# Optimization experiments

Hardware: AMD Instinct MI355X
Metric: run time of the kernel (lower is better)

The kernel has to match this reference:

```python
import jax, jax.numpy as jnp
import numpy as np

B = 256        # number of graphs
NPG = 256      # nodes per graph
N = B * NPG    # total nodes
F = 128        # node feature dim
DEG = 16       # avg degree
E = N * DEG    # total edges
LAT = [32, 32, 32, 1]
D = sum(LAT)   # total_latent_dim = 97
K = 30         # sortpool k
C1, C2, KW2 = 16, 32, 5
DENSE = ((K - 2) // 2 + 1 - KW2 + 1) * C2  # 352
OUT = 2


def setup_inputs() -> dict:
    key = jax.random.key(0)
    ks = jax.random.split(key, 16)
    node_feat = jax.random.normal(ks[0], (N, F), jnp.float32)
    # edges constrained within each graph (block-diagonal adjacency)
    base = ((jnp.arange(E, dtype=jnp.int32) // (E // B)) * NPG).astype(jnp.int32)
    src = jax.random.randint(ks[1], (E,), 0, NPG, dtype=jnp.int32) + base
    dst = jax.random.randint(ks[2], (E,), 0, NPG, dtype=jnp.int32) + base
    degs = jnp.zeros((N,), jnp.int32).at[dst].add(1)  # in-degree per node
    s = 0.1
    dims = [F] + LAT
    inp = {"node_feat": node_feat, "src": src, "dst": dst, "degs": degs}
    for i in range(4):
        inp[f"W{i}"] = jax.random.normal(ks[3 + i], (dims[i], dims[i + 1]), jnp.float32) * s
        inp[f"b{i}"] = jnp.zeros((dims[i + 1],), jnp.float32)
    inp["conv1_w"] = jax.random.normal(ks[8], (C1, 1, D), jnp.float32) * s
    inp["conv1_b"] = jnp.zeros((C1,), jnp.float32)
    inp["conv2_w"] = jax.random.normal(ks[9], (C2, C1, KW2), jnp.float32) * s
    inp["conv2_b"] = jnp.zeros((C2,), jnp.float32)
    inp["out_w"] = jax.random.normal(ks[10], (DENSE, OUT), jnp.float32) * s
    inp["out_b"] = jnp.zeros((OUT,), jnp.float32)
    return inp


def reference(node_feat, W0, b0, W1, b1, W2, b2, W3, b3,
              conv1_w, conv1_b, conv2_w, conv2_b, out_w, out_b,
              src, dst, degs):
    n = node_feat.shape[0]
    deg1 = (degs.astype(node_feat.dtype) + 1.0)[:, None]  # node_degs = deg + 1
    h = node_feat
    feats = []
    for W, b in ((W0, b0), (W1, b1), (W2, b2), (W3, b3)):
        # gnn_spmm(n2n, h) + h : sparse adjacency matmul via segment add
        pooled = jnp.zeros((n, h.shape[1]), h.dtype).at[dst].add(h[src]) + h
        h = jnp.tanh((pooled @ W + b) / deg1)
        feats.append(h)
    Z = jnp.concatenate(feats, axis=1)          # [N, D]
    Zb = Z.reshape(B, NPG, D)                   # equal-sized graphs
    # sortpooling: top-k on last latent channel per graph, gather rows
    _, idx = jax.lax.top_k(Zb[:, :, -1], K)     # [B, K]
    sp = jnp.take_along_axis(Zb, idx[:, :, None], axis=1)  # [B, K, D]
    x = sp.reshape(B, 1, K * D)
    dn = ('NCH', 'OIH', 'NCH')
    x = jax.lax.conv_general_dilated(x, conv1_w, (D,), 'VALID', dimension_numbers=dn)
    x = jax.nn.relu(x + conv1_b[None, :, None])          # [B, C1, K]
    x = x.reshape(B, C1, K // 2, 2).max(axis=-1)         # maxpool1d(2,2) -> [B, C1, 15]
    x = jax.lax.conv_general_dilated(x, conv2_w, (1,), 'VALID', dimension_numbers=dn)
    x = jax.nn.relu(x + conv2_b[None, :, None])          # [B, C2, 11]
    to_dense = x.reshape(B, -1)                          # [B, 352]
    out = jax.nn.relu(to_dense @ out_w + out_b)
    return jax.nn.relu(out)  # original applies conv1d_activation twice at the end
```

## Files before the change

### kernel.cpp

```cpp
#include <hip/hip_runtime.h>

#define NPG  256
#define EPG  4096
#define FDIM 128
#define KTOP 30

__global__ __launch_bounds__(256, 1)
void dgcnn_fused(const float* __restrict__ node_feat,
                 const int* __restrict__ srcv, const int* __restrict__ dstv,
                 const int* __restrict__ degs,
                 const float* __restrict__ W0, const float* __restrict__ b0,
                 const float* __restrict__ W1, const float* __restrict__ b1,
                 const float* __restrict__ W2, const float* __restrict__ b2,
                 const float* __restrict__ W3, const float* __restrict__ b3,
                 const float* __restrict__ cw1, const float* __restrict__ cb1,
                 const float* __restrict__ cw2, const float* __restrict__ cb2,
                 const float* __restrict__ ow,  const float* __restrict__ ob,
                 float* __restrict__ outp)
{
    __shared__ float Ybuf[NPG * 33];
    __shared__ int   srclist[EPG];
    __shared__ int   offs[NPG];
    __shared__ int   cnt [NPG];
    __shared__ int   degl[NPG];
    __shared__ float invd[NPG];
    __shared__ float keys[NPG];
    __shared__ int   sel [KTOP + 2];

    const int g = blockIdx.x;
    const int t = threadIdx.x;

    int dn = degs[g * NPG + t];
    degl[t] = dn;
    cnt[t]  = 0;
    invd[t] = 1.0f / (float)(dn + 1);
    offs[t] = dn;
    __syncthreads();
    for (int s = 1; s < NPG; s <<= 1) {
        int v = (t >= s) ? offs[t - s] : 0;
        __syncthreads();
        offs[t] += v;
        __syncthreads();
    }
    int excl = offs[t] - dn;
    __syncthreads();
    offs[t] = excl;
    __syncthreads();
    {
        const int* sg = srcv + g * EPG;
        const int* dg = dstv + g * EPG;
        for (int i = 0; i < EPG / NPG; i++) {
            int e  = t + i * NPG;
            int ss = sg[e] & (NPG - 1);
            int dd = dg[e] & (NPG - 1);
            int p  = atomicAdd(&cnt[dd], 1);
            srclist[offs[dd] + p] = ss;
        }
    }

    float acc[32];
    #pragma unroll
    for (int c = 0; c < 32; c++) acc[c] = 0.f;
    {
        const float* nf = node_feat + (size_t)g * NPG * FDIM;
        for (int kc = 0; kc < 4; kc++) {
            __syncthreads();
            #pragma unroll
            for (int i = 0; i < 8; i++) {
                int Fi = t + i * 256;
                int n  = Fi >> 3, k4 = Fi & 7;
                const float4 v = *(const float4*)(nf + n * FDIM + kc * 32 + k4 * 4);
                float* p = &Ybuf[n * 33 + k4 * 4];
                p[0] = v.x; p[1] = v.y; p[2] = v.z; p[3] = v.w;
            }
            __syncthreads();
            #pragma unroll
            for (int k = 0; k < 32; k++) {
                float h = Ybuf[t * 33 + k];
                const float* wr = W0 + (kc * 32 + k) * 32;
                #pragma unroll
                for (int c = 0; c < 32; c++) acc[c] = fmaf(h, wr[c], acc[c]);
            }
        }
        __syncthreads();
        #pragma unroll
        for (int c = 0; c < 32; c++) Ybuf[t * 33 + c] = acc[c];
        __syncthreads();
    }

    float h1[32], h2[32], h3[32];
    const float iv = invd[t];
    const int   o  = offs[t];
    const int   d  = degl[t];

    auto agg = [&](float (&h)[32]) {
        #pragma unroll
        for (int c = 0; c < 32; c++) h[c] = Ybuf[t * 33 + c];
        for (int j = 0; j < d; j++) {
            int a = srclist[o + j];
            const float* yr = &Ybuf[a * 33];
            #pragma unroll
            for (int c = 0; c < 32; c++) h[c] += yr[c];
        }
    };
    auto act = [&](float (&h)[32], const float* bb) {
        #pragma unroll
        for (int c = 0; c < 32; c++) h[c] = tanhf((h[c] + bb[c]) * iv);
    };
    auto matml = [&](const float (&h)[32], const float* Wn) {
        float a[32];
        #pragma unroll
        for (int c = 0; c < 32; c++) a[c] = 0.f;
        #pragma unroll
        for (int k = 0; k < 32; k++) {
            const float* wr = Wn + k * 32;
            float hk = h[k];
            #pragma unroll
            for (int c = 0; c < 32; c++) a[c] = fmaf(hk, wr[c], a[c]);
        }
        __syncthreads();
        #pragma unroll
        for (int c = 0; c < 32; c++) Ybuf[t * 33 + c] = a[c];
        __syncthreads();
    };

    agg(h1); act(h1, b0); matml(h1, W1);
    agg(h2); act(h2, b1); matml(h2, W2);
    agg(h3); act(h3, b2);
    {
        float a3 = 0.f;
        #pragma unroll
        for (int k = 0; k < 32; k++) a3 = fmaf(h3[k], W3[k], a3);
        __syncthreads();
        Ybuf[t * 33] = a3;
        __syncthreads();
    }
    float kv;
    {
        float s = Ybuf[t * 33];
        for (int j = 0; j < d; j++) s += Ybuf[srclist[o + j] * 33];
        kv = tanhf((s + b3[0]) * iv);
        keys[t] = kv;
    }
    __syncthreads();

    int rank = 0;
    #pragma unroll 4
    for (int j = 0; j < NPG; j++) {
        float vj = keys[j];
        rank += ((vj > kv) || ((vj == kv) && (j < t))) ? 1 : 0;
    }
    if (rank < KTOP) sel[rank] = t;
    __syncthreads();

    float* sp    = (float*)srclist;
    float* x1    = sp + 30 * 97;
    float* xp    = x1 + 480;
    float* dense = xp + 240;

    if (rank < KTOP) {
        float* dp = sp + rank * 97;
        #pragma unroll
        for (int c = 0; c < 32; c++) dp[c]      = h1[c];
        #pragma unroll
        for (int c = 0; c < 32; c++) dp[32 + c] = h2[c];
        #pragma unroll
        for (int c = 0; c < 32; c++) dp[64 + c] = h3[c];
        dp[96] = kv;
    }
    __syncthreads();

    for (int idx = t; idx < 480; idx += 256) {
        int k = idx >> 4, c = idx & 15;
        float s = cb1[c];
        for (int dd = 0; dd < 97; dd++) s = fmaf(sp[k * 97 + dd], cw1[c * 97 + dd], s);
        x1[c * 30 + k] = fmaxf(s, 0.f);
    }
    __syncthreads();
    for (int idx = t; idx < 240; idx += 256) {
        int c = idx / 15, k = idx - c * 15;
        xp[idx] = fmaxf(x1[c * 30 + 2 * k], x1[c * 30 + 2 * k + 1]);
    }
    __syncthreads();
    for (int idx = t; idx < 352; idx += 256) {
        int c = idx / 11, j = idx - c * 11;
        float s = cb2[c];
        for (int i2 = 0; i2 < 16; i2++) {
            #pragma unroll
            for (int tt = 0; tt < 5; tt++)
                s = fmaf(xp[i2 * 15 + j + tt], cw2[(c * 16 + i2) * 5 + tt], s);
        }
        dense[idx] = fmaxf(s, 0.f);
    }
    __syncthreads();
    if (t < 64) {
        float a0 = 0.f, a1 = 0.f;
        for (int dd = t; dd < 352; dd += 64) {
            float v = dense[dd];
            a0 = fmaf(v, ow[dd * 2],     a0);
            a1 = fmaf(v, ow[dd * 2 + 1], a1);
        }
        #pragma unroll
        for (int off2 = 32; off2 > 0; off2 >>= 1) {
            a0 += __shfl_down(a0, off2);
            a1 += __shfl_down(a1, off2);
        }
        if (t == 0) {
            outp[g * 2 + 0] = fmaxf(a0 + ob[0], 0.f);
            outp[g * 2 + 1] = fmaxf(a1 + ob[1], 0.f);
        }
    }
}

extern "C" void kernel_launch(void* const* d_in, const int* in_sizes, int n_in,
                              void* d_out, int out_size, void* d_ws, size_t ws_size,
                              hipStream_t stream) {
    const float* node_feat = (const float*)d_in[0];
    const int*   src       = (const int*)  d_in[1];
    const int*   dst       = (const int*)  d_in[2];
    const int*   degsp     = (const int*)  d_in[3];
    const float* W0 = (const float*)d_in[4];
    const float* b0 = (const float*)d_in[5];
    const float* W1 = (const float*)d_in[6];
    const float* b1 = (const float*)d_in[7];
    const float* W2 = (const float*)d_in[8];
    const float* b2 = (const float*)d_in[9];
    const float* W3 = (const float*)d_in[10];
    const float* b3 = (const float*)d_in[11];
    const float* cw1 = (const float*)d_in[12];
    const float* cb1 = (const float*)d_in[13];
    const float* cw2 = (const float*)d_in[14];
    const float* cb2 = (const float*)d_in[15];
    const float* ow  = (const float*)d_in[16];
    const float* ob  = (const float*)d_in[17];

    dgcnn_fused<<<dim3(256), dim3(256), 0, stream>>>(
        node_feat, src, dst, degsp,
        W0, b0, W1, b1, W2, b2, W3, b3,
        cw1, cb1, cw2, cb2, ow, ob, (float*)d_out);
}
```

Measured before the change: 181.8 us.

## Split node features across two thread halves with 512-thread blocks

Doubles the block to 512 threads so that each node is handled by two threads, each owning 16 feature channels in aggregation and half of the K dimension in the matmuls. Partial matmul results are combined through shared memory in two synchronized phases. The degree prefix scan becomes a wavefront shuffle scan, and the first-layer input is loaded straight into registers instead of being staged through shared memory. The aim is more parallelism and latency hiding with 256 blocks on the device, at the cost of extra barriers and a duplicated scalar-key aggregation.

```diff
diff --git a/kernel.cpp b/kernel.cpp
--- a/kernel.cpp
+++ b/kernel.cpp
@@ -5,7 +5,7 @@
 #define FDIM 128
 #define KTOP 30
 
-__global__ __launch_bounds__(256, 1)
+__global__ __launch_bounds__(512, 2)
 void dgcnn_fused(const float* __restrict__ node_feat,
                  const int* __restrict__ srcv, const int* __restrict__ dstv,
                  const int* __restrict__ degs,
@@ -25,32 +25,46 @@
     __shared__ int   degl[NPG];
     __shared__ float invd[NPG];
     __shared__ float keys[NPG];
-    __shared__ int   sel [KTOP + 2];
-
-    const int g = blockIdx.x;
-    const int t = threadIdx.x;
-
-    int dn = degs[g * NPG + t];
-    degl[t] = dn;
-    cnt[t]  = 0;
-    invd[t] = 1.0f / (float)(dn + 1);
-    offs[t] = dn;
-    __syncthreads();
-    for (int s = 1; s < NPG; s <<= 1) {
-        int v = (t >= s) ? offs[t - s] : 0;
-        __syncthreads();
-        offs[t] += v;
-        __syncthreads();
-    }
-    int excl = offs[t] - dn;
-    __syncthreads();
-    offs[t] = excl;
-    __syncthreads();
+    __shared__ int   wsum[4];
+
+    const int g    = blockIdx.x;
+    const int t    = threadIdx.x;
+    const int n    = t & (NPG - 1);
+    const int half = t >> 8;
+    const int co   = half * 16;
+
+    const int dn = degs[g * NPG + n];
+    if (half == 0) {
+        degl[n] = dn;
+        cnt[n]  = 0;
+        invd[n] = 1.0f / (float)(dn + 1);
+    }
+    {
+        int v = (half == 0) ? dn : 0;
+        const int lane = t & 63;
+        #pragma unroll
+        for (int off = 1; off < 64; off <<= 1) {
+            int u = __shfl_up(v, off);
+            if (lane >= off) v += u;
+        }
+        if (half == 0 && lane == 63) wsum[t >> 6] = v;
+        __syncthreads();
+        if (half == 0) {
+            const int w = t >> 6;
+            int base = 0;
+            #pragma unroll
+            for (int i = 0; i < 4; i++) base += (i < w) ? wsum[i] : 0;
+            offs[n] = base + v - dn;
+        }
+        __syncthreads();
+    }
+
     {
         const int* sg = srcv + g * EPG;
         const int* dg = dstv + g * EPG;
-        for (int i = 0; i < EPG / NPG; i++) {
-            int e  = t + i * NPG;
+        #pragma unroll
+        for (int i = 0; i < EPG / 512; i++) {
+            int e  = t + i * 512;
             int ss = sg[e] & (NPG - 1);
             int dd = dg[e] & (NPG - 1);
             int p  = atomicAdd(&cnt[dd], 1);
@@ -58,89 +72,101 @@
         }
     }
 
-    float acc[32];
-    #pragma unroll
-    for (int c = 0; c < 32; c++) acc[c] = 0.f;
-    {
-        const float* nf = node_feat + (size_t)g * NPG * FDIM;
-        for (int kc = 0; kc < 4; kc++) {
-            __syncthreads();
-            #pragma unroll
-            for (int i = 0; i < 8; i++) {
-                int Fi = t + i * 256;
-                int n  = Fi >> 3, k4 = Fi & 7;
-                const float4 v = *(const float4*)(nf + n * FDIM + kc * 32 + k4 * 4);
-                float* p = &Ybuf[n * 33 + k4 * 4];
-                p[0] = v.x; p[1] = v.y; p[2] = v.z; p[3] = v.w;
+    {
+        const float* nf = node_feat + ((size_t)g * NPG + n) * FDIM + half * 64;
+        float4 rv[16];
+        #pragma unroll
+        for (int i = 0; i < 16; i++) rv[i] = ((const float4*)nf)[i];
+
+        float acc[32];
+        #pragma unroll
+        for (int c = 0; c < 32; c++) acc[c] = 0.f;
+        #pragma unroll
+        for (int kk = 0; kk < 16; kk++) {
+            const float hx[4] = {rv[kk].x, rv[kk].y, rv[kk].z, rv[kk].w};
+            #pragma unroll
+            for (int q = 0; q < 4; q++) {
+                const float* wr = W0 + (half * 64 + kk * 4 + q) * 32;
+                const float  hk = hx[q];
+                #pragma unroll
+                for (int c = 0; c < 32; c++) acc[c] = fmaf(hk, wr[c], acc[c]);
             }
-            __syncthreads();
-            #pragma unroll
-            for (int k = 0; k < 32; k++) {
-                float h = Ybuf[t * 33 + k];
-                const float* wr = W0 + (kc * 32 + k) * 32;
-                #pragma unroll
-                for (int c = 0; c < 32; c++) acc[c] = fmaf(h, wr[c], acc[c]);
-            }
-        }
-        __syncthreads();
-        #pragma unroll
-        for (int c = 0; c < 32; c++) Ybuf[t * 33 + c] = acc[c];
-        __syncthreads();
-    }
-
-    float h1[32], h2[32], h3[32];
-    const float iv = invd[t];
-    const int   o  = offs[t];
-    const int   d  = degl[t];
-
-    auto agg = [&](float (&h)[32]) {
-        #pragma unroll
-        for (int c = 0; c < 32; c++) h[c] = Ybuf[t * 33 + c];
+        }
+        __syncthreads();
+        if (half == 0) {
+            #pragma unroll
+            for (int c = 0; c < 32; c++) Ybuf[n * 33 + c] = acc[c];
+        }
+        __syncthreads();
+        if (half == 1) {
+            #pragma unroll
+            for (int c = 0; c < 32; c++) Ybuf[n * 33 + c] += acc[c];
+        }
+        __syncthreads();
+    }
+
+    const float iv = invd[n];
+    const int   o  = offs[n];
+    const int   d  = degl[n];
+
+    auto agg16 = [&](float (&h)[16]) {
+        const float* self = &Ybuf[n * 33 + co];
+        #pragma unroll
+        for (int c = 0; c < 16; c++) h[c] = self[c];
         for (int j = 0; j < d; j++) {
-            int a = srclist[o + j];
-            const float* yr = &Ybuf[a * 33];
-            #pragma unroll
-            for (int c = 0; c < 32; c++) h[c] += yr[c];
+            const float* yr = &Ybuf[srclist[o + j] * 33 + co];
+            #pragma unroll
+            for (int c = 0; c < 16; c++) h[c] += yr[c];
         }
     };
-    auto act = [&](float (&h)[32], const float* bb) {
-        #pragma unroll
-        for (int c = 0; c < 32; c++) h[c] = tanhf((h[c] + bb[c]) * iv);
+    auto act16 = [&](float (&h)[16], const float* bb) {
+        #pragma unroll
+        for (int c = 0; c < 16; c++) h[c] = tanhf((h[c] + bb[co + c]) * iv);
     };
-    auto matml = [&](const float (&h)[32], const float* Wn) {
+    auto matml16 = [&](const float (&h)[16], const float* Wn) {
         float a[32];
         #pragma unroll
         for (int c = 0; c < 32; c++) a[c] = 0.f;
         #pragma unroll
-        for (int k = 0; k < 32; k++) {
-            const float* wr = Wn + k * 32;
-            float hk = h[k];
+        for (int kk = 0; kk < 16; kk++) {
+            const float* wr = Wn + (co + kk) * 32;
+            const float  hk = h[kk];
             #pragma unroll
             for (int c = 0; c < 32; c++) a[c] = fmaf(hk, wr[c], a[c]);
         }
         __syncthreads();
-        #pragma unroll
-        for (int c = 0; c < 32; c++) Ybuf[t * 33 + c] = a[c];
+        if (half == 0) {
+            #pragma unroll
+            for (int c = 0; c < 32; c++) Ybuf[n * 33 + c] = a[c];
+        }
+        __syncthreads();
+        if (half == 1) {
+            #pragma unroll
+            for (int c = 0; c < 32; c++) Ybuf[n * 33 + c] += a[c];
+        }
         __syncthreads();
     };
 
-    agg(h1); act(h1, b0); matml(h1, W1);
-    agg(h2); act(h2, b1); matml(h2, W2);
-    agg(h3); act(h3, b2);
+    float h1[16], h2[16], h3[16];
+    agg16(h1); act16(h1, b0); matml16(h1, W1);
+    agg16(h2); act16(h2, b1); matml16(h2, W2);
+    agg16(h3); act16(h3, b2);
     {
         float a3 = 0.f;
         #pragma unroll
-        for (int k = 0; k < 32; k++) a3 = fmaf(h3[k], W3[k], a3);
-        __syncthreads();
-        Ybuf[t * 33] = a3;
+        for (int kk = 0; kk < 16; kk++) a3 = fmaf(h3[kk], W3[co + kk], a3);
+        __syncthreads();
+        if (half == 0) Ybuf[n * 33] = a3;
+        __syncthreads();
+        if (half == 1) Ybuf[n * 33] += a3;
         __syncthreads();
     }
     float kv;
     {
-        float s = Ybuf[t * 33];
+        float s = Ybuf[n * 33];
         for (int j = 0; j < d; j++) s += Ybuf[srclist[o + j] * 33];
         kv = tanhf((s + b3[0]) * iv);
-        keys[t] = kv;
+        if (half == 0) keys[n] = kv;
     }
     __syncthreads();
 
@@ -148,10 +174,8 @@
     #pragma unroll 4
     for (int j = 0; j < NPG; j++) {
         float vj = keys[j];
-        rank += ((vj > kv) || ((vj == kv) && (j < t))) ? 1 : 0;
-    }
-    if (rank < KTOP) sel[rank] = t;
-    __syncthreads();
+        rank += ((vj > kv) || ((vj == kv) && (j < n))) ? 1 : 0;
+    }
 
     float* sp    = (float*)srclist;
     float* x1    = sp + 30 * 97;
@@ -159,30 +183,30 @@
     float* dense = xp + 240;
 
     if (rank < KTOP) {
-        float* dp = sp + rank * 97;
-        #pragma unroll
-        for (int c = 0; c < 32; c++) dp[c]      = h1[c];
-        #pragma unroll
-        for (int c = 0; c < 32; c++) dp[32 + c] = h2[c];
-        #pragma unroll
-        for (int c = 0; c < 32; c++) dp[64 + c] = h3[c];
-        dp[96] = kv;
-    }
-    __syncthreads();
-
-    for (int idx = t; idx < 480; idx += 256) {
+        float* dp = sp + rank * 97 + co;
+        #pragma unroll
+        for (int c = 0; c < 16; c++) dp[c]      = h1[c];
+        #pragma unroll
+        for (int c = 0; c < 16; c++) dp[32 + c] = h2[c];
+        #pragma unroll
+        for (int c = 0; c < 16; c++) dp[64 + c] = h3[c];
+        if (half == 0) sp[rank * 97 + 96] = kv;
+    }
+    __syncthreads();
+
+    for (int idx = t; idx < 480; idx += 512) {
         int k = idx >> 4, c = idx & 15;
         float s = cb1[c];
         for (int dd = 0; dd < 97; dd++) s = fmaf(sp[k * 97 + dd], cw1[c * 97 + dd], s);
         x1[c * 30 + k] = fmaxf(s, 0.f);
     }
     __syncthreads();
-    for (int idx = t; idx < 240; idx += 256) {
+    for (int idx = t; idx < 240; idx += 512) {
         int c = idx / 15, k = idx - c * 15;
         xp[idx] = fmaxf(x1[c * 30 + 2 * k], x1[c * 30 + 2 * k + 1]);
     }
     __syncthreads();
-    for (int idx = t; idx < 352; idx += 256) {
+    for (int idx = t; idx < 352; idx += 512) {
         int c = idx / 11, j = idx - c * 11;
         float s = cb2[c];
         for (int i2 = 0; i2 < 16; i2++) {
@@ -234,7 +258,7 @@
     const float* ow  = (const float*)d_in[16];
     const float* ob  = (const float*)d_in[17];
 
-    dgcnn_fused<<<dim3(256), dim3(256), 0, stream>>>(
+    dgcnn_fused<<<dim3(256), dim3(512), 0, stream>>>(
         node_feat, src, dst, degsp,
         W0, b0, W1, b1, W2, b2, W3, b3,
         cw1, cb1, cw2, cb2, ow, ob, (float*)d_out);
```

Result: slower. 224.2 us (+23.3%).
